# Performance work log

Measured on AMD Instinct MI355X. Metric: run time of the kernel, lower is better.

The kernel has to match this reference:

```python
import jax, jax.numpy as jnp
import numpy as np

B, S, D = 8, 2048, 128
NEG = -1e9

def setup_inputs() -> dict:
    key = jax.random.key(0)
    kq, kk, kv = jax.random.split(key, 3)
    query = jax.random.normal(kq, (B, S, D), dtype=jnp.float32)
    k_ = jax.random.normal(kk, (B, S, D), dtype=jnp.float32)
    value = jax.random.normal(kv, (B, S, D), dtype=jnp.float32)
    mask = jnp.tril(jnp.ones((S, S), dtype=jnp.int32))  # causal (seq_len, seq_len)
    return {"query": query, "key": k_, "value": value, "mask": mask}

def reference(query, key, value, mask):
    d_k = query.shape[-1]
    # scores: [B, S, S]
    scores = jnp.einsum('bqd,bkd->bqk', query, key) / jnp.sqrt(jnp.asarray(d_k, jnp.float32))
    scores = jnp.where(mask == 0, jnp.asarray(NEG, scores.dtype), scores)
    p_attn = jax.nn.softmax(scores, axis=-1)
    # dropout p=0.0 -> identity
    return jnp.einsum('bqk,bkd->bqd', p_attn, value)
```

## Files before the change

### kernel.cpp

```cpp
#include <hip/hip_runtime.h>


#define BATCH 8
#define SEQ   2048
#define DIM   128
#define CK    256

typedef _Float16 v4h __attribute__((ext_vector_type(4)));
typedef _Float16 v8h __attribute__((ext_vector_type(8)));
typedef float    v4f __attribute__((ext_vector_type(4)));

#define QF_H 0u
#define KF_H 2097152u
#define VF_H 4194304u
#define OP_H 6291456u
#define ML_B 31457280u
#define WS_NEED 31752192u

__constant__ const float kScale = 0.08838834764831845f;

__global__ __launch_bounds__(256) void prepass(
    const float* __restrict__ K, const float* __restrict__ V,
    _Float16* __restrict__ wsh)
{
    const int b = blockIdx.x;
    const int t = threadIdx.x;
    if (b < 1024) {
        __shared__ float tile[16][132];
        const int batch = b >> 7, vt = b & 127;
        const float* src = V + ((size_t)batch * SEQ + vt * 16) * DIM;
        const int row = t >> 4, col = (t & 15) * 8;
        *(v4f*)&tile[row][col]     = *(const v4f*)(src + (size_t)row * DIM + col);
        *(v4f*)&tile[row][col + 4] = *(const v4f*)(src + (size_t)row * DIM + col + 4);
        __syncthreads();
        const int n = t >> 4, p = (t >> 2) & 3, qd = t & 3;
        v8h h;
        #pragma unroll
        for (int j = 0; j < 8; ++j) {
            const int d  = 32 * p + 16 * (j >> 2) + n;
            const int kk = qd * 4 + (j & 3);
            h[j] = (_Float16)tile[kk][d];
        }
        const int w = n * 64 + ((p * 16 + qd * 4) ^ ((n & 7) << 2));
        *(v8h*)(wsh + VF_H + (size_t)batch * 262144 + vt * 2048 + w * 2) = h;
    } else {
        const int i = (b - 1024) * 256 + t;
        const int seg = i & 15, row = i >> 4;
        const float* src = K + (size_t)row * DIM + seg * 8;
        v4f a = *(const v4f*)src;
        v4f c = *(const v4f*)(src + 4);
        v8h h;
        #pragma unroll
        for (int j = 0; j < 4; ++j) {
            h[j]     = (_Float16)a[j];
            h[j + 4] = (_Float16)c[j];
        }
        const int w = (seg * 4) ^ ((row & 7) << 2);
        *(v8h*)(wsh + KF_H + (size_t)row * DIM + w * 2) = h;
    }
}

__device__ __forceinline__ void dma16(const _Float16* g, const _Float16* l) {
    __builtin_amdgcn_global_load_lds(
        (const __attribute__((address_space(1))) unsigned int*)g,
        (__attribute__((address_space(3))) unsigned int*)(unsigned int)(uintptr_t)l,
        16, 0, 0);
}

__global__ __launch_bounds__(256, 4) void attn_chunk(
    const float* __restrict__ Q, const _Float16* __restrict__ wsh,
    float* __restrict__ Ml, _Float16* __restrict__ Op)
{
    __shared__ __align__(16) _Float16 lds[16384];

    const int batch = blockIdx.x & 7;
    int g = blockIdx.x >> 3;
    int c = 0;
    for (; c < 8; ++c) { const int cnt = 32 - 4 * c; if (g < cnt) break; g -= cnt; }
    const int wave = threadIdx.x >> 6;
    const int qt = 16 * c + g * 4 + wave;
    const int q0 = qt * 16;
    const int kbeg = c * CK;

    const int lane = threadIdx.x & 63;
    const int n = lane & 15, quad = lane >> 4;
    const size_t bo = (size_t)batch * SEQ * DIM;

    const _Float16* Kf = wsh + KF_H + bo;
    const _Float16* Vf = wsh + VF_H + bo;

    v8h qa[4];
    {
        const float* qp = Q + bo + (size_t)(q0 + n) * DIM + quad * 8;
        #pragma unroll
        for (int p = 0; p < 4; ++p) {
            v4f a = *(const v4f*)(qp + p * 32);
            v4f b2 = *(const v4f*)(qp + p * 32 + 4);
            v8h h;
            #pragma unroll
            for (int j = 0; j < 4; ++j) {
                h[j]     = (_Float16)(a[j] * kScale);
                h[j + 4] = (_Float16)(b2[j] * kScale);
            }
            qa[p] = h;
        }
    }

    const _Float16* gseg = ((wave < 2) ? (Kf + (size_t)kbeg * DIM)
                                       : (Vf + (size_t)(kbeg >> 4) * 2048))
                           + (wave & 1) * 2048;
    const int ldsseg = (wave >> 1) * 4096 + (wave & 1) * 2048;

    int koff[4];
    #pragma unroll
    for (int p = 0; p < 4; ++p)
        koff[p] = n * 128 + (((quad * 4 + p * 16) ^ ((n & 7) << 2)) << 1);

    float l_run = 0.0f;
    v4f of[8];
    #pragma unroll
    for (int dc = 0; dc < 8; ++dc) of[dc] = (v4f){0.f, 0.f, 0.f, 0.f};

    const int qn0 = q0 + n - kbeg;
    const int kq = quad * 4;

    #pragma unroll
    for (int i = 0; i < 4; ++i)
        dma16(gseg + i * 512 + lane * 8, &lds[ldsseg + i * 512]);

    #pragma unroll
    for (int kb = 0; kb < 8; ++kb) {
        __syncthreads();
        if (kb < 7) {
            const _Float16* gs = gseg + (kb + 1) * 4096;
            const int lb = ((kb + 1) & 1) * 8192 + ldsseg;
            #pragma unroll
            for (int i = 0; i < 4; ++i)
                dma16(gs + i * 512 + lane * 8, &lds[lb + i * 512]);
        }
        const int base = (kb & 1) * 8192;
        #pragma unroll
        for (int t16 = 0; t16 < 2; ++t16) {
            v4f s = (v4f){0.f, 0.f, 0.f, 0.f};
            #pragma unroll
            for (int p = 0; p < 4; ++p) {
                v8h kf = *(const v8h*)&lds[base + t16 * 2048 + koff[p]];
                s = __builtin_amdgcn_mfma_f32_16x16x32_f16(kf, qa[p], s, 0, 0, 0);
            }
            v4h pf;
            float ps = 0.f;
            #pragma unroll
            for (int r = 0; r < 4; ++r) {
                const float sv = (kb * 32 + t16 * 16 + kq + r > qn0) ? -1e30f : s[r];
                const float p = __expf(sv);
                ps += p;
                pf[r] = (_Float16)p;
            }
            l_run += ps;
            #pragma unroll
            for (int p = 0; p < 4; ++p) {
                v8h vv = *(const v8h*)&lds[base + 4096 + t16 * 2048 + koff[p]];
                v4h vlo = __builtin_shufflevector(vv, vv, 0, 1, 2, 3);
                v4h vhi = __builtin_shufflevector(vv, vv, 4, 5, 6, 7);
                of[2 * p]     = __builtin_amdgcn_mfma_f32_16x16x16f16(vlo, pf, of[2 * p], 0, 0, 0);
                of[2 * p + 1] = __builtin_amdgcn_mfma_f32_16x16x16f16(vhi, pf, of[2 * p + 1], 0, 0, 0);
            }
        }
    }

    l_run += __shfl_xor(l_run, 16);
    l_run += __shfl_xor(l_run, 32);

    const int rs = (2048 * c - 128 * c * (c - 1)) * 8
                 + batch * (2048 - CK * c) + (q0 + n - CK * c);
    _Float16* op = (_Float16*)(wsh + OP_H) + (size_t)rs * DIM
                 - (size_t)0;
    op = Op + (size_t)rs * DIM;
    #pragma unroll
    for (int dc = 0; dc < 8; ++dc) {
        v4h o;
        #pragma unroll
        for (int r = 0; r < 4; ++r) o[r] = (_Float16)of[dc][r];
        *(v4h*)(op + dc * 16 + quad * 4) = o;
    }
    if (quad == 0) Ml[rs] = l_run;
}

__global__ __launch_bounds__(256) void combine(
    const _Float16* __restrict__ Op, const float* __restrict__ Ml,
    float* __restrict__ O)
{
    const int gid = blockIdx.x * 256 + threadIdx.x;
    const size_t e = (size_t)gid * 4;
    const int d = (int)(e & 127);
    const int q = (int)((e >> 7) & 2047);
    const int b = (int)(e >> 18);
    const int nc = (q >> 8) + 1;
    float L = 0.f;
    v4f acc = (v4f){0.f, 0.f, 0.f, 0.f};
    for (int c = 0; c < nc; ++c) {
        const int rs = (2048 * c - 128 * c * (c - 1)) * 8 + b * (2048 - 256 * c) + (q - 256 * c);
        L += Ml[rs];
        v4h o = *(const v4h*)(Op + (size_t)rs * DIM + d);
        #pragma unroll
        for (int r = 0; r < 4; ++r) acc[r] += (float)o[r];
    }
    const float rl = 1.0f / L;
    *(v4f*)(O + e) = acc * rl;
}

__global__ __launch_bounds__(128) void attn_fwd(
    const float* __restrict__ Q, const float* __restrict__ K,
    const float* __restrict__ V, float* __restrict__ O)
{
    const int batch = blockIdx.x & 7;
    const int qb    = blockIdx.x >> 3;
    const int tid   = threadIdx.x;
    const int wave  = tid >> 6;
    const int lane  = tid & 63;
    const int n     = lane & 15;
    const int quad  = lane >> 4;

    const int q0      = qb * 32 + wave * 16;
    const int my_last = qb * 2 + wave;
    const int nt      = qb * 2 + 2;

    const size_t bo = (size_t)batch * SEQ * DIM;

    __shared__ __align__(16) _Float16 Ks[16 * 136];
    __shared__ __align__(16) _Float16 Vt[128 * 20];
    typedef _Float16 v2h __attribute__((ext_vector_type(2)));

    v4h qf[8];
    {
        const float* qp = Q + bo + (size_t)(q0 + n) * DIM + quad * 4;
        #pragma unroll
        for (int dc = 0; dc < 8; ++dc) {
            v4f qv = *(const v4f*)(qp + dc * 16);
            v4h h;
            #pragma unroll
            for (int i = 0; i < 4; ++i) h[i] = (_Float16)(qv[i] * kScale);
            qf[dc] = h;
        }
    }

    float m_run = -1e30f, l_run = 0.0f;
    v4f of[8];
    #pragma unroll
    for (int dc = 0; dc < 8; ++dc) of[dc] = (v4f){0.f, 0.f, 0.f, 0.f};

    const int krow = tid >> 3;
    const int kcol = (tid & 7) * 16;
    const int vr   = (tid >> 4) * 2;
    const int vc   = (tid & 15) * 4;

    for (int tk = 0; tk < nt; ++tk) {
        const int k0 = tk * 16;
        {
            const float* kp = K + bo + (size_t)(k0 + krow) * DIM + kcol;
            v4f k0v = *(const v4f*)(kp);
            v4f k1v = *(const v4f*)(kp + 4);
            v4f k2v = *(const v4f*)(kp + 8);
            v4f k3v = *(const v4f*)(kp + 12);
            const float* vp = V + bo + (size_t)(k0 + vr) * DIM + vc;
            v4f va0 = *(const v4f*)(vp);
            v4f va1 = *(const v4f*)(vp + DIM);
            v4f vb0 = *(const v4f*)(vp + 64);
            v4f vb1 = *(const v4f*)(vp + DIM + 64);

            v8h h0, h1;
            #pragma unroll
            for (int i = 0; i < 4; ++i) {
                h0[i]     = (_Float16)k0v[i];
                h0[i + 4] = (_Float16)k1v[i];
                h1[i]     = (_Float16)k2v[i];
                h1[i + 4] = (_Float16)k3v[i];
            }
            *(v8h*)&Ks[krow * 136 + kcol]     = h0;
            *(v8h*)&Ks[krow * 136 + kcol + 8] = h1;

            #pragma unroll
            for (int i = 0; i < 4; ++i) {
                v2h p0 = { (_Float16)va0[i], (_Float16)va1[i] };
                v2h p1 = { (_Float16)vb0[i], (_Float16)vb1[i] };
                *(v2h*)&Vt[(vc + i) * 20 + vr]      = p0;
                *(v2h*)&Vt[(vc + 64 + i) * 20 + vr] = p1;
            }
        }
        __syncthreads();

        if (tk <= my_last) {
            v4f s = (v4f){0.f, 0.f, 0.f, 0.f};
            #pragma unroll
            for (int dc = 0; dc < 8; ++dc) {
                v4h kf = *(const v4h*)&Ks[n * 136 + dc * 16 + quad * 4];
                s = __builtin_amdgcn_mfma_f32_16x16x16f16(kf, qf[dc], s, 0, 0, 0);
            }
            if (tk == my_last) {
                #pragma unroll
                for (int r = 0; r < 4; ++r)
                    if (quad * 4 + r > n) s[r] = -1e30f;
            }
            float tm = fmaxf(fmaxf(s[0], s[1]), fmaxf(s[2], s[3]));
            tm = fmaxf(tm, __shfl_xor(tm, 16));
            tm = fmaxf(tm, __shfl_xor(tm, 32));
            const float m_new = fmaxf(m_run, tm);
            const float alpha = __expf(m_run - m_new);
            v4f p;
            #pragma unroll
            for (int r = 0; r < 4; ++r) p[r] = __expf(s[r] - m_new);
            float ps = p[0] + p[1] + p[2] + p[3];
            ps += __shfl_xor(ps, 16);
            ps += __shfl_xor(ps, 32);
            l_run = l_run * alpha + ps;
            m_run = m_new;

            v4h pf;
            #pragma unroll
            for (int r = 0; r < 4; ++r) pf[r] = (_Float16)p[r];

            #pragma unroll
            for (int dc = 0; dc < 8; ++dc) {
                v4h vf = *(const v4h*)&Vt[(dc * 16 + n) * 20 + quad * 4];
                of[dc] *= alpha;
                of[dc] = __builtin_amdgcn_mfma_f32_16x16x16f16(vf, pf, of[dc], 0, 0, 0);
            }
        }
        __syncthreads();
    }

    const float rl = 1.0f / l_run;
    float* op = O + bo + (size_t)(q0 + n) * DIM + quad * 4;
    #pragma unroll
    for (int dc = 0; dc < 8; ++dc) {
        v4f o = of[dc] * rl;
        *(v4f*)(op + dc * 16) = o;
    }
}

extern "C" void kernel_launch(void* const* d_in, const int* in_sizes, int n_in,
                              void* d_out, int out_size, void* d_ws, size_t ws_size,
                              hipStream_t stream) {
    const float* Q = (const float*)d_in[0];
    const float* K = (const float*)d_in[1];
    const float* V = (const float*)d_in[2];
    float* Out = (float*)d_out;

    if (ws_size >= (size_t)WS_NEED) {
        _Float16* wsh = (_Float16*)d_ws;
        _Float16* Op  = wsh + OP_H;
        float*    Ml  = (float*)((char*)d_ws + ML_B);
        prepass<<<dim3(2048), dim3(256), 0, stream>>>(K, V, wsh);
        attn_chunk<<<dim3(8 * 144), dim3(256), 0, stream>>>(Q, wsh, Ml, Op);
        combine<<<dim3(2048), dim3(256), 0, stream>>>(Op, Ml, Out);
    } else {
        attn_fwd<<<dim3(BATCH * (SEQ / 32)), dim3(128), 0, stream>>>(Q, K, V, Out);
    }
}
```

Measured before the change: 112.6 us.

## Register-block two query tiles per wave to reuse LDS K/V fragments

Each wave now computes two 16-row query tiles instead of one, and the block shrinks from four waves to two, so each block still covers the same 64 query rows. Every K and V fragment read from LDS now feeds two MFMAs instead of one, which halves LDS read traffic per unit of matrix work and gives more independent MFMA chains to hide latency. Each wave also issues twice as many async global-to-LDS copies. The cost is roughly double the accumulator and Q registers per wave, and the launch bound drops to 128 threads with a minimum of 3 blocks, which may lower occupancy.

```diff
diff --git a/kernel.cpp b/kernel.cpp
--- a/kernel.cpp
+++ b/kernel.cpp
@@ -67,7 +67,7 @@
         16, 0, 0);
 }
 
-__global__ __launch_bounds__(256, 4) void attn_chunk(
+__global__ __launch_bounds__(128, 3) void attn_chunk(
     const float* __restrict__ Q, const _Float16* __restrict__ wsh,
     float* __restrict__ Ml, _Float16* __restrict__ Op)
 {
@@ -78,7 +78,7 @@
     int c = 0;
     for (; c < 8; ++c) { const int cnt = 32 - 4 * c; if (g < cnt) break; g -= cnt; }
     const int wave = threadIdx.x >> 6;
-    const int qt = 16 * c + g * 4 + wave;
+    const int qt = 16 * c + g * 4 + 2 * wave;
     const int q0 = qt * 16;
     const int kbeg = c * CK;
 
@@ -89,9 +89,10 @@
     const _Float16* Kf = wsh + KF_H + bo;
     const _Float16* Vf = wsh + VF_H + bo;
 
-    v8h qa[4];
-    {
-        const float* qp = Q + bo + (size_t)(q0 + n) * DIM + quad * 8;
+    v8h qa[2][4];
+    #pragma unroll
+    for (int u = 0; u < 2; ++u) {
+        const float* qp = Q + bo + (size_t)(q0 + 16 * u + n) * DIM + quad * 8;
         #pragma unroll
         for (int p = 0; p < 4; ++p) {
             v4f a = *(const v4f*)(qp + p * 32);
@@ -102,30 +103,31 @@
                 h[j]     = (_Float16)(a[j] * kScale);
                 h[j + 4] = (_Float16)(b2[j] * kScale);
             }
-            qa[p] = h;
-        }
-    }
-
-    const _Float16* gseg = ((wave < 2) ? (Kf + (size_t)kbeg * DIM)
-                                       : (Vf + (size_t)(kbeg >> 4) * 2048))
-                           + (wave & 1) * 2048;
-    const int ldsseg = (wave >> 1) * 4096 + (wave & 1) * 2048;
+            qa[u][p] = h;
+        }
+    }
+
+    const _Float16* gseg = (wave == 0) ? (Kf + (size_t)kbeg * DIM)
+                                       : (Vf + (size_t)(kbeg >> 4) * 2048);
+    const int ldsseg = wave * 4096;
 
     int koff[4];
     #pragma unroll
     for (int p = 0; p < 4; ++p)
         koff[p] = n * 128 + (((quad * 4 + p * 16) ^ ((n & 7) << 2)) << 1);
 
-    float l_run = 0.0f;
-    v4f of[8];
-    #pragma unroll
-    for (int dc = 0; dc < 8; ++dc) of[dc] = (v4f){0.f, 0.f, 0.f, 0.f};
+    float l_run[2] = {0.0f, 0.0f};
+    v4f of[2][8];
+    #pragma unroll
+    for (int u = 0; u < 2; ++u)
+        #pragma unroll
+        for (int dc = 0; dc < 8; ++dc) of[u][dc] = (v4f){0.f, 0.f, 0.f, 0.f};
 
     const int qn0 = q0 + n - kbeg;
     const int kq = quad * 4;
 
     #pragma unroll
-    for (int i = 0; i < 4; ++i)
+    for (int i = 0; i < 8; ++i)
         dma16(gseg + i * 512 + lane * 8, &lds[ldsseg + i * 512]);
 
     #pragma unroll
@@ -135,55 +137,66 @@
             const _Float16* gs = gseg + (kb + 1) * 4096;
             const int lb = ((kb + 1) & 1) * 8192 + ldsseg;
             #pragma unroll
-            for (int i = 0; i < 4; ++i)
+            for (int i = 0; i < 8; ++i)
                 dma16(gs + i * 512 + lane * 8, &lds[lb + i * 512]);
         }
         const int base = (kb & 1) * 8192;
         #pragma unroll
         for (int t16 = 0; t16 < 2; ++t16) {
-            v4f s = (v4f){0.f, 0.f, 0.f, 0.f};
+            v4f s0 = (v4f){0.f, 0.f, 0.f, 0.f};
+            v4f s1 = (v4f){0.f, 0.f, 0.f, 0.f};
             #pragma unroll
             for (int p = 0; p < 4; ++p) {
                 v8h kf = *(const v8h*)&lds[base + t16 * 2048 + koff[p]];
-                s = __builtin_amdgcn_mfma_f32_16x16x32_f16(kf, qa[p], s, 0, 0, 0);
-            }
-            v4h pf;
-            float ps = 0.f;
-            #pragma unroll
-            for (int r = 0; r < 4; ++r) {
-                const float sv = (kb * 32 + t16 * 16 + kq + r > qn0) ? -1e30f : s[r];
-                const float p = __expf(sv);
-                ps += p;
-                pf[r] = (_Float16)p;
-            }
-            l_run += ps;
+                s0 = __builtin_amdgcn_mfma_f32_16x16x32_f16(kf, qa[0][p], s0, 0, 0, 0);
+                s1 = __builtin_amdgcn_mfma_f32_16x16x32_f16(kf, qa[1][p], s1, 0, 0, 0);
+            }
+            v4h pf[2];
+            #pragma unroll
+            for (int u = 0; u < 2; ++u) {
+                const v4f s = u ? s1 : s0;
+                const int qn = qn0 + 16 * u;
+                float ps = 0.f;
+                #pragma unroll
+                for (int r = 0; r < 4; ++r) {
+                    const float sv = (kb * 32 + t16 * 16 + kq + r > qn) ? -1e30f : s[r];
+                    const float p = __expf(sv);
+                    ps += p;
+                    pf[u][r] = (_Float16)p;
+                }
+                l_run[u] += ps;
+            }
             #pragma unroll
             for (int p = 0; p < 4; ++p) {
                 v8h vv = *(const v8h*)&lds[base + 4096 + t16 * 2048 + koff[p]];
                 v4h vlo = __builtin_shufflevector(vv, vv, 0, 1, 2, 3);
                 v4h vhi = __builtin_shufflevector(vv, vv, 4, 5, 6, 7);
-                of[2 * p]     = __builtin_amdgcn_mfma_f32_16x16x16f16(vlo, pf, of[2 * p], 0, 0, 0);
-                of[2 * p + 1] = __builtin_amdgcn_mfma_f32_16x16x16f16(vhi, pf, of[2 * p + 1], 0, 0, 0);
-            }
-        }
-    }
-
-    l_run += __shfl_xor(l_run, 16);
-    l_run += __shfl_xor(l_run, 32);
-
-    const int rs = (2048 * c - 128 * c * (c - 1)) * 8
-                 + batch * (2048 - CK * c) + (q0 + n - CK * c);
-    _Float16* op = (_Float16*)(wsh + OP_H) + (size_t)rs * DIM
-                 - (size_t)0;
-    op = Op + (size_t)rs * DIM;
-    #pragma unroll
-    for (int dc = 0; dc < 8; ++dc) {
-        v4h o;
-        #pragma unroll
-        for (int r = 0; r < 4; ++r) o[r] = (_Float16)of[dc][r];
-        *(v4h*)(op + dc * 16 + quad * 4) = o;
-    }
-    if (quad == 0) Ml[rs] = l_run;
+                of[0][2 * p]     = __builtin_amdgcn_mfma_f32_16x16x16f16(vlo, pf[0], of[0][2 * p], 0, 0, 0);
+                of[0][2 * p + 1] = __builtin_amdgcn_mfma_f32_16x16x16f16(vhi, pf[0], of[0][2 * p + 1], 0, 0, 0);
+                of[1][2 * p]     = __builtin_amdgcn_mfma_f32_16x16x16f16(vlo, pf[1], of[1][2 * p], 0, 0, 0);
+                of[1][2 * p + 1] = __builtin_amdgcn_mfma_f32_16x16x16f16(vhi, pf[1], of[1][2 * p + 1], 0, 0, 0);
+            }
+        }
+    }
+
+    #pragma unroll
+    for (int u = 0; u < 2; ++u) {
+        float l = l_run[u];
+        l += __shfl_xor(l, 16);
+        l += __shfl_xor(l, 32);
+
+        const int rs = (2048 * c - 128 * c * (c - 1)) * 8
+                     + batch * (2048 - CK * c) + (q0 + 16 * u + n - CK * c);
+        _Float16* op = Op + (size_t)rs * DIM;
+        #pragma unroll
+        for (int dc = 0; dc < 8; ++dc) {
+            v4h o;
+            #pragma unroll
+            for (int r = 0; r < 4; ++r) o[r] = (_Float16)of[u][dc][r];
+            *(v4h*)(op + dc * 16 + quad * 4) = o;
+        }
+        if (quad == 0) Ml[rs] = l;
+    }
 }
 
 __global__ __launch_bounds__(256) void combine(
@@ -351,7 +364,7 @@
         _Float16* Op  = wsh + OP_H;
         float*    Ml  = (float*)((char*)d_ws + ML_B);
         prepass<<<dim3(2048), dim3(256), 0, stream>>>(K, V, wsh);
-        attn_chunk<<<dim3(8 * 144), dim3(256), 0, stream>>>(Q, wsh, Ml, Op);
+        attn_chunk<<<dim3(8 * 144), dim3(128), 0, stream>>>(Q, wsh, Ml, Op);
         combine<<<dim3(2048), dim3(256), 0, stream>>>(Op, Ml, Out);
     } else {
         attn_fwd<<<dim3(BATCH * (SEQ / 32)), dim3(128), 0, stream>>>(Q, K, V, Out);
```

Measured after the change: 126.1 us. +11.9%, slower.
